# Kernel optimization log

Hardware: AMD Instinct MI355X
Metric: run time of the kernel (lower is better)

Reference implementation:

```python
import jax, jax.numpy as jnp
import numpy as np

B, T, I, H, O, P = 32, 8192, 16, 128, 3, 1024


def setup_inputs() -> dict:
    key = jax.random.key(0)
    ks = jax.random.split(key, 8)
    x = jax.random.normal(ks[0], (B, T, I), dtype=jnp.float32)
    # feature channel 2 holds the photo id (original code does x[:,:,2].long())
    ids = jax.random.randint(ks[1], (B, T), 0, P)
    x = x.at[:, :, 2].set(ids.astype(jnp.float32))
    s = 1.0 / np.sqrt(H).astype(np.float32)
    W_ih = jax.random.uniform(ks[2], (4 * H, I), minval=-s, maxval=s, dtype=jnp.float32)
    W_hh = jax.random.uniform(ks[3], (4 * H, H), minval=-s, maxval=s, dtype=jnp.float32)
    b_ih = jax.random.uniform(ks[4], (4 * H,), minval=-s, maxval=s, dtype=jnp.float32)
    b_hh = jax.random.uniform(ks[5], (4 * H,), minval=-s, maxval=s, dtype=jnp.float32)
    W_fc = jax.random.uniform(ks[6], (O, H), minval=-s, maxval=s, dtype=jnp.float32)
    b_fc = jax.random.uniform(ks[7], (O,), minval=-s, maxval=s, dtype=jnp.float32)
    return dict(x=x, W_ih=W_ih, W_hh=W_hh, b_ih=b_ih, b_hh=b_hh,
                W_fc=W_fc, b_fc=b_fc, num_photos=P)


def _lstm(x, W_ih, W_hh, b_ih, b_hh):
    # single-layer batch_first LSTM, PyTorch gate order (i, f, g, o), zero init state
    Bz = x.shape[0]
    Hh = W_hh.shape[1]
    # precompute input contribution for all timesteps: [B, T, 4H]
    xg = jnp.einsum('bti,gi->btg', x, W_ih) + b_ih + b_hh

    def step(carry, gx):
        h, c = carry
        g = gx + h @ W_hh.T
        i, f, gg, o = jnp.split(g, 4, axis=-1)
        i = jax.nn.sigmoid(i)
        f = jax.nn.sigmoid(f)
        gg = jnp.tanh(gg)
        o = jax.nn.sigmoid(o)
        c = f * c + i * gg
        h = o * jnp.tanh(c)
        return (h, c), h

    h0 = jnp.zeros((Bz, Hh), x.dtype)
    _, hs = jax.lax.scan(step, (h0, h0), jnp.swapaxes(xg, 0, 1))  # [T, B, H]
    return jnp.swapaxes(hs, 0, 1)  # [B, T, H]


def reference(x, W_ih, W_hh, b_ih, b_hh, W_fc, b_fc, num_photos):
    Bz, T, _ = x.shape
    h = _lstm(x, W_ih, W_hh, b_ih, b_hh)          # [B, T, H]
    out = h @ W_fc.T + b_fc                        # [B, T, 3]
    ids = x[:, :, 2].astype(jnp.int32)             # [B, T]
    valid = ids < num_photos
    safe = jnp.where(valid, ids, 0)
    # flatten (batch, photo_id) into a single segment id per element
    seg = (jnp.arange(Bz, dtype=jnp.int32)[:, None] * num_photos + safe).reshape(-1)
    w = valid.astype(out.dtype)
    sums = jax.ops.segment_sum((out * w[..., None]).reshape(-1, out.shape[-1]),
                               seg, num_segments=Bz * num_photos)
    sums = sums.reshape(Bz, num_photos, out.shape[-1])
    counts = jax.ops.segment_sum(w.reshape(-1), seg, num_segments=Bz * num_photos)
    counts = counts.reshape(Bz, num_photos, 1)
    counts = jnp.where(counts == 0, 1.0, counts)   # matches photo_counts[photo_counts==0]=1
    return sums / counts
```

## Files before the change

kernel.cpp:

```cpp
#include <hip/hip_runtime.h>

#define B_ 32
#define T_ 8192
#define I_ 16
#define H_ 128
#define P_ 1024
#define O_ 3

#define REP8(M) M(0) M(1) M(2) M(3) M(4) M(5) M(6) M(7)
#define FORG(M, n) M(0, n) M(1, n) M(2, n) M(3, n)
#define FORALLW(M) FORG(M,0) FORG(M,1) FORG(M,2) FORG(M,3) \
                   FORG(M,4) FORG(M,5) FORG(M,6) FORG(M,7)

#define DPPF(v, ctrl) \
    __int_as_float(__builtin_amdgcn_mov_dpp(__float_as_int(v), (ctrl), 0xF, 0xF, true))
#define SWZF(v, imm) \
    __int_as_float(__builtin_amdgcn_ds_swizzle(__float_as_int(v), (imm)))

__device__ __forceinline__ float tanh_f(float x) {
    return 2.f / (1.f + __expf(-2.f * x)) - 1.f;
}

__device__ __forceinline__ void lds_barrier() {
    asm volatile("s_waitcnt lgkmcnt(0)\n\ts_barrier" ::: "memory");
}

__global__ __launch_bounds__(512) __attribute__((amdgpu_waves_per_eu(2, 2)))
void lstm_fused(
    const float* __restrict__ x,
    const float* __restrict__ W_ih,
    const float* __restrict__ W_hh,
    const float* __restrict__ b_ih,
    const float* __restrict__ b_hh,
    const float* __restrict__ W_fc,
    float* __restrict__ sums,
    float* __restrict__ counts)
{
    const int b   = blockIdx.x;
    const int tid = threadIdx.x;
    const int j   = tid >> 2;
    const int kc  = tid & 3;

    __shared__ __align__(16) float h_s[2][H_];
    __shared__ __align__(16) float x_tile[2][16*I_];
    __shared__ float sums_lds[P_ * O_];
    __shared__ float counts_lds[P_];

    const float4* wp0 = (const float4*)(W_hh + (0 * H_ + j) * H_ + kc * 32);
    const float4* wp1 = (const float4*)(W_hh + (1 * H_ + j) * H_ + kc * 32);
    const float4* wp2 = (const float4*)(W_hh + (2 * H_ + j) * H_ + kc * 32);
    const float4* wp3 = (const float4*)(W_hh + (3 * H_ + j) * H_ + kc * 32);
    #define WLOAD(g, n) float wx##g##_##n, wy##g##_##n, wz##g##_##n, ww##g##_##n; \
        { float4 t_ = wp##g[n]; wx##g##_##n = t_.x; wy##g##_##n = t_.y; \
          wz##g##_##n = t_.z; ww##g##_##n = t_.w; }
    FORALLW(WLOAD)
    #define WPIN(g, n) asm volatile( \
        "v_mov_b32 %0,%0\n\tv_mov_b32 %1,%1\n\tv_mov_b32 %2,%2\n\tv_mov_b32 %3,%3" \
        : "+v"(wx##g##_##n), "+v"(wy##g##_##n), "+v"(wz##g##_##n), "+v"(ww##g##_##n));
    FORALLW(WPIN)

    float4 u0 = *(const float4*)(W_ih + (0 * H_ + j) * I_ + kc * 4);
    float4 u1 = *(const float4*)(W_ih + (1 * H_ + j) * I_ + kc * 4);
    float4 u2 = *(const float4*)(W_ih + (2 * H_ + j) * I_ + kc * 4);
    float4 u3 = *(const float4*)(W_ih + (3 * H_ + j) * I_ + kc * 4);
    asm volatile("v_mov_b32 %0,%0\n\tv_mov_b32 %1,%1\n\tv_mov_b32 %2,%2\n\tv_mov_b32 %3,%3"
                 : "+v"(u0.x), "+v"(u0.y), "+v"(u0.z), "+v"(u0.w));
    asm volatile("v_mov_b32 %0,%0\n\tv_mov_b32 %1,%1\n\tv_mov_b32 %2,%2\n\tv_mov_b32 %3,%3"
                 : "+v"(u1.x), "+v"(u1.y), "+v"(u1.z), "+v"(u1.w));
    asm volatile("v_mov_b32 %0,%0\n\tv_mov_b32 %1,%1\n\tv_mov_b32 %2,%2\n\tv_mov_b32 %3,%3"
                 : "+v"(u2.x), "+v"(u2.y), "+v"(u2.z), "+v"(u2.w));
    asm volatile("v_mov_b32 %0,%0\n\tv_mov_b32 %1,%1\n\tv_mov_b32 %2,%2\n\tv_mov_b32 %3,%3"
                 : "+v"(u3.x), "+v"(u3.y), "+v"(u3.z), "+v"(u3.w));

    const float bias = b_ih[kc * H_ + j] + b_hh[kc * H_ + j];
    const float wfc  = (kc < 3) ? W_fc[kc * H_ + j] : 0.f;

    for (int i = tid; i < P_ * O_; i += 512) sums_lds[i] = 0.f;
    for (int i = tid; i < P_;      i += 512) counts_lds[i] = 0.f;
    if (tid < H_) h_s[0][tid] = 0.f;

    const float* xb = x + (size_t)b * T_ * I_;
    float4 xr4 = make_float4(0.f, 0.f, 0.f, 0.f);
    if (tid < 64) {
        xr4 = ((const float4*)xb)[tid];
        ((float4*)&x_tile[0][0])[tid] = xr4;
    }
    float c = 0.f;
    __syncthreads();

    #pragma unroll 1
    for (int t = 0; t < T_; ++t) {
        const int off = t & 15;
        const int btx = (t >> 4) & 1;
        const int bh  = t & 1;

        if (tid < 64) {
            if (off == 0 && t + 16 < T_)
                xr4 = ((const float4*)(xb + (t + 16) * I_))[tid];
            if (off == 8 && t + 8 < T_)
                ((float4*)&x_tile[btx ^ 1][0])[tid] = xr4;
        }

        const float4 xv = *(const float4*)&x_tile[btx][off * I_ + kc * 4];
        const int    id = (int)x_tile[btx][off * I_ + 2];

        float acc0 = 0.f, acc1 = 0.f, acc2 = 0.f, acc3 = 0.f;
        const float4* hc = (const float4*)&h_s[bh][kc * 32];
        #define HFMA(n) { float4 hv = hc[n]; \
            acc0 = fmaf(hv.x, wx0_##n, acc0); acc0 = fmaf(hv.y, wy0_##n, acc0); \
            acc0 = fmaf(hv.z, wz0_##n, acc0); acc0 = fmaf(hv.w, ww0_##n, acc0); \
            acc1 = fmaf(hv.x, wx1_##n, acc1); acc1 = fmaf(hv.y, wy1_##n, acc1); \
            acc1 = fmaf(hv.z, wz1_##n, acc1); acc1 = fmaf(hv.w, ww1_##n, acc1); \
            acc2 = fmaf(hv.x, wx2_##n, acc2); acc2 = fmaf(hv.y, wy2_##n, acc2); \
            acc2 = fmaf(hv.z, wz2_##n, acc2); acc2 = fmaf(hv.w, ww2_##n, acc2); \
            acc3 = fmaf(hv.x, wx3_##n, acc3); acc3 = fmaf(hv.y, wy3_##n, acc3); \
            acc3 = fmaf(hv.z, wz3_##n, acc3); acc3 = fmaf(hv.w, ww3_##n, acc3); }
        REP8(HFMA)
        acc0 = fmaf(xv.x, u0.x, acc0); acc0 = fmaf(xv.y, u0.y, acc0);
        acc0 = fmaf(xv.z, u0.z, acc0); acc0 = fmaf(xv.w, u0.w, acc0);
        acc1 = fmaf(xv.x, u1.x, acc1); acc1 = fmaf(xv.y, u1.y, acc1);
        acc1 = fmaf(xv.z, u1.z, acc1); acc1 = fmaf(xv.w, u1.w, acc1);
        acc2 = fmaf(xv.x, u2.x, acc2); acc2 = fmaf(xv.y, u2.y, acc2);
        acc2 = fmaf(xv.z, u2.z, acc2); acc2 = fmaf(xv.w, u2.w, acc2);
        acc3 = fmaf(xv.x, u3.x, acc3); acc3 = fmaf(xv.y, u3.y, acc3);
        acc3 = fmaf(xv.z, u3.z, acc3); acc3 = fmaf(xv.w, u3.w, acc3);

        float s_;
        s_ = DPPF(acc0, 0xB1); acc0 += s_;
        s_ = DPPF(acc1, 0xB1); acc1 += s_;
        s_ = DPPF(acc2, 0xB1); acc2 += s_;
        s_ = DPPF(acc3, 0xB1); acc3 += s_;
        s_ = DPPF(acc0, 0x4E); acc0 += s_;
        s_ = DPPF(acc1, 0x4E); acc1 += s_;
        s_ = DPPF(acc2, 0x4E); acc2 += s_;
        s_ = DPPF(acc3, 0x4E); acc3 += s_;

        float tg = (kc == 0) ? acc0 : (kc == 1) ? acc1 : (kc == 2) ? acc2 : acc3;
        tg += bias;
        const bool  isg = (kc == 2);
        const float arg = isg ? (tg + tg) : tg;
        const float sf  = 1.f / (1.f + __expf(-arg));
        const float act = isg ? (sf + sf - 1.f) : sf;

        const float gi = DPPF(act, 0x00);
        const float gf = DPPF(act, 0x55);
        const float gg = DPPF(act, 0xAA);
        const float go = DPPF(act, 0xFF);
        c = fmaf(gf, c, gi * gg);
        const float hnew = go * tanh_f(c);

        if (kc == 0) h_s[bh ^ 1][j] = hnew;

        float p = hnew * wfc;
        p += SWZF(p, 0x101F);
        p += SWZF(p, 0x201F);
        p += SWZF(p, 0x401F);
        const bool idv = ((unsigned)id < P_);
        const int  l   = tid & 63;
        if (((l & 28) == 0) && kc < 3 && idv)
            atomicAdd(&sums_lds[id * O_ + kc], p);
        if (tid == 0 && idv)
            atomicAdd(&counts_lds[id], 1.f);

        lds_barrier();
    }

    float* sums_g = sums + (size_t)b * P_ * O_;
    for (int i = tid; i < P_ * O_; i += 512) sums_g[i] = sums_lds[i];
    float* cnt_g = counts + (size_t)b * P_;
    for (int i = tid; i < P_; i += 512) cnt_g[i] = counts_lds[i];
}

__global__ void finalize_kernel(const float* __restrict__ sums,
                                const float* __restrict__ counts,
                                const float* __restrict__ b_fc,
                                float* __restrict__ out)
{
    const int idx = blockIdx.x * blockDim.x + threadIdx.x;
    if (idx >= B_ * P_ * O_) return;
    const int o  = idx % O_;
    const int bp = idx / O_;
    const float cnt = counts[bp];
    const float denom = (cnt > 0.f) ? cnt : 1.f;
    out[idx] = (sums[idx] + cnt * b_fc[o]) / denom;
}

extern "C" void kernel_launch(void* const* d_in, const int* in_sizes, int n_in,
                              void* d_out, int out_size, void* d_ws, size_t ws_size,
                              hipStream_t stream) {
    const float* x    = (const float*)d_in[0];
    const float* W_ih = (const float*)d_in[1];
    const float* W_hh = (const float*)d_in[2];
    const float* b_ih = (const float*)d_in[3];
    const float* b_hh = (const float*)d_in[4];
    const float* W_fc = (const float*)d_in[5];
    const float* b_fc = (const float*)d_in[6];

    float* out    = (float*)d_out;
    float* sums   = (float*)d_ws;
    float* counts = sums + (size_t)B_ * P_ * O_;

    lstm_fused<<<B_, 512, 0, stream>>>(x, W_ih, W_hh, b_ih, b_hh, W_fc, sums, counts);

    const int n = B_ * P_ * O_;
    finalize_kernel<<<(n + 255) / 256, 256, 0, stream>>>(sums, counts, b_fc, out);
}
```

Measured before the change: 6.871 ms.

## Use fp16 packed dot2 for the LSTM recurrent matvec and fewer atomics

```diff
diff --git a/kernel.cpp b/kernel.cpp
--- a/kernel.cpp
+++ b/kernel.cpp
@@ -7,10 +7,26 @@
 #define P_ 1024
 #define O_ 3
 
-#define REP8(M) M(0) M(1) M(2) M(3) M(4) M(5) M(6) M(7)
-#define FORG(M, n) M(0, n) M(1, n) M(2, n) M(3, n)
-#define FORALLW(M) FORG(M,0) FORG(M,1) FORG(M,2) FORG(M,3) \
-                   FORG(M,4) FORG(M,5) FORG(M,6) FORG(M,7)
+typedef _Float16 h2 __attribute__((ext_vector_type(2)));
+typedef _Float16 h4 __attribute__((ext_vector_type(4)));
+typedef _Float16 h8 __attribute__((ext_vector_type(8)));
+
+#if __has_builtin(__builtin_amdgcn_fdot2)
+#define FDOT2(a, b, c) __builtin_amdgcn_fdot2((a), (b), (c), false)
+#else
+__device__ __forceinline__ float fdot2_asm(h2 a, h2 b, float c) {
+    asm("v_dot2_f32_f16 %0, %1, %2, %0" : "+v"(c) : "v"(a), "v"(b));
+    return c;
+}
+#define FDOT2(a, b, c) fdot2_asm((a), (b), (c))
+#endif
+
+#define FORME(M, g) M(g,0,0) M(g,0,1) M(g,0,2) M(g,0,3) \
+                    M(g,1,0) M(g,1,1) M(g,1,2) M(g,1,3) \
+                    M(g,2,0) M(g,2,1) M(g,2,2) M(g,2,3) \
+                    M(g,3,0) M(g,3,1) M(g,3,2) M(g,3,3)
+#define FORALL(M) FORME(M,0) FORME(M,1) FORME(M,2) FORME(M,3)
+#define FORG(M) M(0) M(1) M(2) M(3)
 
 #define DPPF(v, ctrl) \
     __int_as_float(__builtin_amdgcn_mov_dpp(__float_as_int(v), (ctrl), 0xF, 0xF, true))
@@ -20,12 +36,15 @@
 __device__ __forceinline__ float tanh_f(float x) {
     return 2.f / (1.f + __expf(-2.f * x)) - 1.f;
 }
+__device__ __forceinline__ h4 cvt4(float4 v) {
+    return (h4){(_Float16)v.x, (_Float16)v.y, (_Float16)v.z, (_Float16)v.w};
+}
 
 __device__ __forceinline__ void lds_barrier() {
     asm volatile("s_waitcnt lgkmcnt(0)\n\ts_barrier" ::: "memory");
 }
 
-__global__ __launch_bounds__(512) __attribute__((amdgpu_waves_per_eu(2, 2)))
+__global__ __launch_bounds__(512, 2) __attribute__((amdgpu_waves_per_eu(2, 2)))
 void lstm_fused(
     const float* __restrict__ x,
     const float* __restrict__ W_ih,
@@ -41,49 +60,39 @@
     const int j   = tid >> 2;
     const int kc  = tid & 3;
 
-    __shared__ __align__(16) float h_s[2][H_];
-    __shared__ __align__(16) float x_tile[2][16*I_];
+    __shared__ __align__(16) _Float16 hh[2][H_];
+    __shared__ __align__(16) _Float16 xt[2][16 * I_];
     __shared__ float sums_lds[P_ * O_];
     __shared__ float counts_lds[P_];
 
-    const float4* wp0 = (const float4*)(W_hh + (0 * H_ + j) * H_ + kc * 32);
-    const float4* wp1 = (const float4*)(W_hh + (1 * H_ + j) * H_ + kc * 32);
-    const float4* wp2 = (const float4*)(W_hh + (2 * H_ + j) * H_ + kc * 32);
-    const float4* wp3 = (const float4*)(W_hh + (3 * H_ + j) * H_ + kc * 32);
-    #define WLOAD(g, n) float wx##g##_##n, wy##g##_##n, wz##g##_##n, ww##g##_##n; \
-        { float4 t_ = wp##g[n]; wx##g##_##n = t_.x; wy##g##_##n = t_.y; \
-          wz##g##_##n = t_.z; ww##g##_##n = t_.w; }
-    FORALLW(WLOAD)
-    #define WPIN(g, n) asm volatile( \
-        "v_mov_b32 %0,%0\n\tv_mov_b32 %1,%1\n\tv_mov_b32 %2,%2\n\tv_mov_b32 %3,%3" \
-        : "+v"(wx##g##_##n), "+v"(wy##g##_##n), "+v"(wz##g##_##n), "+v"(ww##g##_##n));
-    FORALLW(WPIN)
-
-    float4 u0 = *(const float4*)(W_ih + (0 * H_ + j) * I_ + kc * 4);
-    float4 u1 = *(const float4*)(W_ih + (1 * H_ + j) * I_ + kc * 4);
-    float4 u2 = *(const float4*)(W_ih + (2 * H_ + j) * I_ + kc * 4);
-    float4 u3 = *(const float4*)(W_ih + (3 * H_ + j) * I_ + kc * 4);
-    asm volatile("v_mov_b32 %0,%0\n\tv_mov_b32 %1,%1\n\tv_mov_b32 %2,%2\n\tv_mov_b32 %3,%3"
-                 : "+v"(u0.x), "+v"(u0.y), "+v"(u0.z), "+v"(u0.w));
-    asm volatile("v_mov_b32 %0,%0\n\tv_mov_b32 %1,%1\n\tv_mov_b32 %2,%2\n\tv_mov_b32 %3,%3"
-                 : "+v"(u1.x), "+v"(u1.y), "+v"(u1.z), "+v"(u1.w));
-    asm volatile("v_mov_b32 %0,%0\n\tv_mov_b32 %1,%1\n\tv_mov_b32 %2,%2\n\tv_mov_b32 %3,%3"
-                 : "+v"(u2.x), "+v"(u2.y), "+v"(u2.z), "+v"(u2.w));
-    asm volatile("v_mov_b32 %0,%0\n\tv_mov_b32 %1,%1\n\tv_mov_b32 %2,%2\n\tv_mov_b32 %3,%3"
-                 : "+v"(u3.x), "+v"(u3.y), "+v"(u3.z), "+v"(u3.w));
+    const float* wr0 = W_hh + (0 * H_ + j) * H_;
+    const float* wr1 = W_hh + (1 * H_ + j) * H_;
+    const float* wr2 = W_hh + (2 * H_ + j) * H_;
+    const float* wr3 = W_hh + (3 * H_ + j) * H_;
+    #define WLOAD(g, m, e) h2 W##g##_##m##_##e = (h2){ \
+        (_Float16)wr##g[kc * 8 + 32 * (m) + 2 * (e)], \
+        (_Float16)wr##g[kc * 8 + 32 * (m) + 2 * (e) + 1]};
+    FORALL(WLOAD)
+
+    #define ULOAD(g) \
+        h2 U##g##_0 = (h2){(_Float16)W_ih[((g) * H_ + j) * I_ + kc * 4 + 0], \
+                           (_Float16)W_ih[((g) * H_ + j) * I_ + kc * 4 + 1]}; \
+        h2 U##g##_1 = (h2){(_Float16)W_ih[((g) * H_ + j) * I_ + kc * 4 + 2], \
+                           (_Float16)W_ih[((g) * H_ + j) * I_ + kc * 4 + 3]};
+    FORG(ULOAD)
 
     const float bias = b_ih[kc * H_ + j] + b_hh[kc * H_ + j];
     const float wfc  = (kc < 3) ? W_fc[kc * H_ + j] : 0.f;
 
     for (int i = tid; i < P_ * O_; i += 512) sums_lds[i] = 0.f;
     for (int i = tid; i < P_;      i += 512) counts_lds[i] = 0.f;
-    if (tid < H_) h_s[0][tid] = 0.f;
+    if (tid < H_) hh[0][tid] = (_Float16)0.f;
 
     const float* xb = x + (size_t)b * T_ * I_;
     float4 xr4 = make_float4(0.f, 0.f, 0.f, 0.f);
     if (tid < 64) {
         xr4 = ((const float4*)xb)[tid];
-        ((float4*)&x_tile[0][0])[tid] = xr4;
+        *(h4*)&xt[0][tid * 4] = cvt4(xr4);
     }
     float c = 0.f;
     __syncthreads();
@@ -98,32 +107,34 @@
             if (off == 0 && t + 16 < T_)
                 xr4 = ((const float4*)(xb + (t + 16) * I_))[tid];
             if (off == 8 && t + 8 < T_)
-                ((float4*)&x_tile[btx ^ 1][0])[tid] = xr4;
+                *(h4*)&xt[btx ^ 1][tid * 4] = cvt4(xr4);
         }
 
-        const float4 xv = *(const float4*)&x_tile[btx][off * I_ + kc * 4];
-        const int    id = (int)x_tile[btx][off * I_ + 2];
+        const h4 xv4 = *(const h4*)&xt[btx][off * I_ + kc * 4];
+        const h2 xv0 = __builtin_shufflevector(xv4, xv4, 0, 1);
+        const h2 xv1 = __builtin_shufflevector(xv4, xv4, 2, 3);
+        const int id = (int)(float)xt[btx][off * I_ + 2];
 
         float acc0 = 0.f, acc1 = 0.f, acc2 = 0.f, acc3 = 0.f;
-        const float4* hc = (const float4*)&h_s[bh][kc * 32];
-        #define HFMA(n) { float4 hv = hc[n]; \
-            acc0 = fmaf(hv.x, wx0_##n, acc0); acc0 = fmaf(hv.y, wy0_##n, acc0); \
-            acc0 = fmaf(hv.z, wz0_##n, acc0); acc0 = fmaf(hv.w, ww0_##n, acc0); \
-            acc1 = fmaf(hv.x, wx1_##n, acc1); acc1 = fmaf(hv.y, wy1_##n, acc1); \
-            acc1 = fmaf(hv.z, wz1_##n, acc1); acc1 = fmaf(hv.w, ww1_##n, acc1); \
-            acc2 = fmaf(hv.x, wx2_##n, acc2); acc2 = fmaf(hv.y, wy2_##n, acc2); \
-            acc2 = fmaf(hv.z, wz2_##n, acc2); acc2 = fmaf(hv.w, ww2_##n, acc2); \
-            acc3 = fmaf(hv.x, wx3_##n, acc3); acc3 = fmaf(hv.y, wy3_##n, acc3); \
-            acc3 = fmaf(hv.z, wz3_##n, acc3); acc3 = fmaf(hv.w, ww3_##n, acc3); }
-        REP8(HFMA)
-        acc0 = fmaf(xv.x, u0.x, acc0); acc0 = fmaf(xv.y, u0.y, acc0);
-        acc0 = fmaf(xv.z, u0.z, acc0); acc0 = fmaf(xv.w, u0.w, acc0);
-        acc1 = fmaf(xv.x, u1.x, acc1); acc1 = fmaf(xv.y, u1.y, acc1);
-        acc1 = fmaf(xv.z, u1.z, acc1); acc1 = fmaf(xv.w, u1.w, acc1);
-        acc2 = fmaf(xv.x, u2.x, acc2); acc2 = fmaf(xv.y, u2.y, acc2);
-        acc2 = fmaf(xv.z, u2.z, acc2); acc2 = fmaf(xv.w, u2.w, acc2);
-        acc3 = fmaf(xv.x, u3.x, acc3); acc3 = fmaf(xv.y, u3.y, acc3);
-        acc3 = fmaf(xv.z, u3.z, acc3); acc3 = fmaf(xv.w, u3.w, acc3);
+        #define HD(m) { \
+            h8 hv = *(const h8*)&hh[bh][kc * 8 + 32 * (m)]; \
+            h2 p0 = __builtin_shufflevector(hv, hv, 0, 1); \
+            h2 p1 = __builtin_shufflevector(hv, hv, 2, 3); \
+            h2 p2 = __builtin_shufflevector(hv, hv, 4, 5); \
+            h2 p3 = __builtin_shufflevector(hv, hv, 6, 7); \
+            acc0 = FDOT2(p0, W0_##m##_0, acc0); acc0 = FDOT2(p1, W0_##m##_1, acc0); \
+            acc0 = FDOT2(p2, W0_##m##_2, acc0); acc0 = FDOT2(p3, W0_##m##_3, acc0); \
+            acc1 = FDOT2(p0, W1_##m##_0, acc1); acc1 = FDOT2(p1, W1_##m##_1, acc1); \
+            acc1 = FDOT2(p2, W1_##m##_2, acc1); acc1 = FDOT2(p3, W1_##m##_3, acc1); \
+            acc2 = FDOT2(p0, W2_##m##_0, acc2); acc2 = FDOT2(p1, W2_##m##_1, acc2); \
+            acc2 = FDOT2(p2, W2_##m##_2, acc2); acc2 = FDOT2(p3, W2_##m##_3, acc2); \
+            acc3 = FDOT2(p0, W3_##m##_0, acc3); acc3 = FDOT2(p1, W3_##m##_1, acc3); \
+            acc3 = FDOT2(p2, W3_##m##_2, acc3); acc3 = FDOT2(p3, W3_##m##_3, acc3); }
+        HD(0) HD(1) HD(2) HD(3)
+        acc0 = FDOT2(xv0, U0_0, acc0); acc0 = FDOT2(xv1, U0_1, acc0);
+        acc1 = FDOT2(xv0, U1_0, acc1); acc1 = FDOT2(xv1, U1_1, acc1);
+        acc2 = FDOT2(xv0, U2_0, acc2); acc2 = FDOT2(xv1, U2_1, acc2);
+        acc3 = FDOT2(xv0, U3_0, acc3); acc3 = FDOT2(xv1, U3_1, acc3);
 
         float s_;
         s_ = DPPF(acc0, 0xB1); acc0 += s_;
@@ -149,16 +160,16 @@
         c = fmaf(gf, c, gi * gg);
         const float hnew = go * tanh_f(c);
 
-        if (kc == 0) h_s[bh ^ 1][j] = hnew;
+        if (kc == 0) hh[bh ^ 1][j] = (_Float16)hnew;
 
         float p = hnew * wfc;
         p += SWZF(p, 0x101F);
         p += SWZF(p, 0x201F);
         p += SWZF(p, 0x401F);
+        p += __shfl_xor(p, 32, 64);
         const bool idv = ((unsigned)id < P_);
-        const int  l   = tid & 63;
-        if (((l & 28) == 0) && kc < 3 && idv)
-            atomicAdd(&sums_lds[id * O_ + kc], p);
+        if (((tid & 63) < 3) && idv)
+            atomicAdd(&sums_lds[id * O_ + (tid & 63)], p);
         if (tid == 0 && idv)
             atomicAdd(&counts_lds[id], 1.f);
 
```

Measured after the change: 6.357 ms. -7.5%, faster.
